# Kernel tuning notes

Measured on AMD Instinct MI355X. Metric: run time of the kernel, lower is better.

The kernel has to match this reference:

```python
import jax, jax.numpy as jnp
import numpy as np

IN_FEATURES = 1024
OUT_FEATURES = 1024
BATCH = 32
SEQ = 1024
EPS = 1e-8


def setup_inputs() -> dict:
    key = jax.random.key(0)
    k1, k2, k3 = jax.random.split(key, 3)
    Efou = jax.random.normal(k1, (BATCH, SEQ, IN_FEATURES), dtype=jnp.float32)
    y = jax.random.normal(k2, (BATCH, IN_FEATURES), dtype=jnp.float32)
    weight = jax.random.normal(k3, (IN_FEATURES, OUT_FEATURES), dtype=jnp.float32)
    return {"Efou": Efou, "y": y, "weight": weight}


def reference(Efou, y, weight):
    # scale = 1/sqrt(in_features)
    scale = 1.0 / np.sqrt(np.float32(weight.shape[0]))
    ys = y * scale  # (b, i) == per-sample column scaling of weight
    # Demodulation norm: sum_i (scale*W[i,o]*y[b,i])^2 = (ys^2) @ (W^2)
    d = jax.lax.rsqrt(jnp.einsum('bi,io->bo', ys * ys, weight * weight) + EPS)  # (b, o)
    # Efou @ (scale*W*y*d) == ((Efou*ys) @ W) * d  -- same math, avoids (b,i,o) weight
    out = jnp.einsum('bsi,io->bso', Efou * ys[:, None, :], weight) * d[:, None, :]
    return out
```

## Files before the change

kernel.cpp:

```cpp
#include <hip/hip_runtime.h>

#define AS1 __attribute__((address_space(1)))
#define AS3 __attribute__((address_space(3)))

typedef __bf16 bf16x8 __attribute__((ext_vector_type(8)));
typedef float f32x4 __attribute__((ext_vector_type(4)));
typedef unsigned short ushort8 __attribute__((ext_vector_type(8)));

__device__ __forceinline__ unsigned short f2bf(float f) {
  union { float f; unsigned u; } v; v.f = f;
  unsigned u = v.u;
  unsigned r = (u + 0x7fffu + ((u >> 16) & 1u)) >> 16;
  return (unsigned short)r;
}

__global__ __launch_bounds__(256) void prep_kernel(const float* __restrict__ y,
                                                   const float* __restrict__ W,
                                                   float* __restrict__ partial,
                                                   unsigned short* __restrict__ WT) {
  __shared__ float ysq[32][32];
  const int o = blockIdx.x * 256 + threadIdx.x;
  const int i0 = blockIdx.y * 32;
  for (int e = threadIdx.x; e < 1024; e += 256) {
    int il = e >> 5, b = e & 31;
    float t = y[b * 1024 + i0 + il] * 0.03125f;
    ysq[il][b] = t * t;
  }
  __syncthreads();

  f32x4 acc[8] = {};
  ushort8 wb[4];
#pragma unroll
  for (int il = 0; il < 32; ++il) {
    float w = W[(size_t)(i0 + il) * 1024 + o];
    wb[il >> 3][il & 7] = f2bf(w);
    float w2 = w * w;
#pragma unroll
    for (int b4 = 0; b4 < 8; ++b4) {
      f32x4 q = *(const f32x4*)&ysq[il][b4 * 4];
#pragma unroll
      for (int k = 0; k < 4; ++k) acc[b4][k] = fmaf(q[k], w2, acc[b4][k]);
    }
  }
  unsigned short* wt = WT + (size_t)o * 1024 + i0;
#pragma unroll
  for (int q = 0; q < 4; ++q) *(ushort8*)(wt + q * 8) = wb[q];
  float* p = partial + (size_t)blockIdx.y * 32768 + o;
#pragma unroll
  for (int b4 = 0; b4 < 8; ++b4)
#pragma unroll
    for (int k = 0; k < 4; ++k) p[(b4 * 4 + k) * 1024] = acc[b4][k];
}

__global__ __launch_bounds__(256) void dcalc_b_kernel(const float* __restrict__ partial,
                                                      float* __restrict__ dmod) {
  const int bo = blockIdx.x * 256 + threadIdx.x;
  float acc = 0.f;
#pragma unroll 8
  for (int is = 0; is < 32; ++is) acc += partial[(size_t)is * 32768 + bo];
  dmod[bo] = rsqrtf(acc + 1e-8f);
}

#define NT 16
#define LDS_TILE 65536

#define BAR __builtin_amdgcn_s_barrier()
#define LGKM0 asm volatile("s_waitcnt lgkmcnt(0)" ::: "memory")
#define VM(n) asm volatile("s_waitcnt vmcnt(" #n ")" ::: "memory")
#define SCHB __builtin_amdgcn_sched_barrier(0)
#define PRIO(x) __builtin_amdgcn_s_setprio(x)

#define STG_B(r, t, dst)                                                     \
  __builtin_amdgcn_global_load_lds(                                          \
      (const AS1 void*)(Ws + (size_t)(r) * 64 * 2048 + (t) * 128),           \
      (AS3 void*)((dst) + 32768 + (r) * 8192 + sldso), 16, 0, 0)

#define A_ISSUE(t)                                                           \
  {                                                                          \
    const float* asrc = Efou + (size_t)(m0 + argp * 4) * 1024 + (t) * 64 + k8; \
    _Pragma("unroll") for (int rr = 0; rr < 4; ++rr) {                       \
      pa[rr][0] = *(const f32x4*)(asrc + rr * 1024);                         \
      pa[rr][1] = *(const f32x4*)(asrc + rr * 1024 + 4);                     \
    }                                                                        \
    yv[0] = *(const f32x4*)(ysS + (t) * 64 + k8);                            \
    yv[1] = *(const f32x4*)(ysS + (t) * 64 + k8 + 4);                        \
  }

#define ACVT_ROW(dst, rr)                                                    \
  {                                                                          \
    const int row = argp * 4 + (rr);                                         \
    bf16x8 ov;                                                               \
    _Pragma("unroll") for (int q = 0; q < 4; ++q) {                          \
      ov[q] = (__bf16)(pa[rr][0][q] * yv[0][q]);                             \
      ov[q + 4] = (__bf16)(pa[rr][1][q] * yv[1][q]);                         \
    }                                                                        \
    *(bf16x8*)((dst) + row * 128 + ((kslot * 16) ^ ((row & 7) << 4))) = ov;  \
  }

#define RD_A(mh, mi, kk)                                                     \
  (*(const bf16x8*)(Ab + (wr * 128 + ((mh) * 4 + (mi)) * 16 + l15) * 128 +   \
                    ((((kk) * 64 + lhi * 16)) ^ swz_rd)))
#define RD_B(nh, ni, kk)                                                     \
  (*(const bf16x8*)(Bb + (wc * 64 + ((nh) * 2 + (ni)) * 16 + l15) * 128 +    \
                    ((((kk) * 64 + lhi * 16)) ^ swz_rd)))

#define LD_A(mh)                                                             \
  { _Pragma("unroll") for (int mi = 0; mi < 4; ++mi)                         \
      _Pragma("unroll") for (int kk = 0; kk < 2; ++kk)                       \
        a[mi][kk] = RD_A(mh, mi, kk); }
#define LD_B_ALL                                                             \
  { _Pragma("unroll") for (int nh = 0; nh < 2; ++nh)                         \
      _Pragma("unroll") for (int ni = 0; ni < 2; ++ni)                       \
        _Pragma("unroll") for (int kk = 0; kk < 2; ++kk)                     \
          bfr[nh][ni][kk] = RD_B(nh, ni, kk); }

#define MM(mh, nh)                                                           \
  do {                                                                       \
    _Pragma("unroll") for (int mi = 0; mi < 4; ++mi)                         \
      _Pragma("unroll") for (int ni = 0; ni < 2; ++ni)                       \
        _Pragma("unroll") for (int kk = 0; kk < 2; ++kk)                     \
          acc[(mh) * 4 + mi][(nh) * 2 + ni] =                                \
              __builtin_amdgcn_mfma_f32_16x16x32_bf16(                       \
                  a[mi][kk], bfr[nh][ni][kk],                                \
                  acc[(mh) * 4 + mi][(nh) * 2 + ni], 0, 0, 0);               \
  } while (0)

__global__ __launch_bounds__(512, 2) void gemmf6_kernel(
    const float* __restrict__ Efou, const float* __restrict__ y,
    const unsigned short* __restrict__ WT, const float* __restrict__ dmod,
    float* __restrict__ out) {
  extern __shared__ char lds[];
  float* ysS = (float*)(lds + 2 * LDS_TILE);

  const int tid = threadIdx.x;
  const int bid = blockIdx.x;
  const int wg = (bid & 7) * 64 + (bid >> 3);
  const int bm = wg >> 2, bn = wg & 3;
  const int m0 = bm * 256, n0 = bn * 256;
  const int b = m0 >> 10;

  const int w = tid >> 6, l = tid & 63;
  const int wr = w >> 2, wc = w & 3;
  const int l15 = l & 15, lhi = l >> 4;
  const int swz_rd = (l15 & 7) << 4;

  const int kslot = tid & 7;
  const int k8 = kslot * 8;
  const int argp = tid >> 3;

  const int srow = tid >> 3;
  const int scb = ((tid & 7) << 4) ^ ((srow & 7) << 4);
  const char* Ws = (const char*)WT + (size_t)(n0 + srow) * 2048 + scb;
  const int sldso = tid * 16;

  f32x4 acc[8][4] = {};
  bf16x8 a[4][2], bfr[2][2][2];
  f32x4 pa[4][2], yv[2];

  {
    float2 yy = *(const float2*)(y + b * 1024 + tid * 2);
    ysS[2 * tid] = yy.x * 0.03125f;
    ysS[2 * tid + 1] = yy.y * 0.03125f;
  }
  __syncthreads();
  {
    char* d0 = lds;
    STG_B(0, 0, d0); STG_B(1, 0, d0); STG_B(2, 0, d0); STG_B(3, 0, d0);
    A_ISSUE(0);
    ACVT_ROW(d0, 0); ACVT_ROW(d0, 1); ACVT_ROW(d0, 2); ACVT_ROW(d0, 3);
  }
  VM(0); LGKM0; BAR;

  for (int t = 0; t < NT - 1; ++t) {
    const char* Ab = lds + (t & 1) * LDS_TILE;
    const char* Bb = Ab + 32768;
    char* dN = lds + ((t & 1) ^ 1) * LDS_TILE;
    const int t1 = t + 1;
    LD_A(0); LD_B_ALL;
    A_ISSUE(t1);
    STG_B(0, t1, dN); STG_B(1, t1, dN); STG_B(2, t1, dN); STG_B(3, t1, dN);
    BAR; LGKM0; SCHB; PRIO(1); MM(0, 0); MM(0, 1); PRIO(0); SCHB; BAR;
    LD_A(1);
    SCHB; PRIO(1);
    ACVT_ROW(dN, 0); ACVT_ROW(dN, 1);
    MM(1, 0);
    ACVT_ROW(dN, 2); ACVT_ROW(dN, 3);
    MM(1, 1);
    PRIO(0); SCHB;
    VM(0);
    LGKM0;
    BAR;
  }

  {
    const char* Ab = lds + ((NT - 1) & 1) * LDS_TILE;
    const char* Bb = Ab + 32768;
    LD_A(0); LD_B_ALL;
    BAR; LGKM0; SCHB; PRIO(1); MM(0, 0); MM(0, 1); PRIO(0); SCHB;
    LD_A(1);
    LGKM0; SCHB; PRIO(1); MM(1, 0); MM(1, 1); PRIO(0); SCHB;
  }

  const int col0 = n0 + wc * 64 + l15;
  float dv[4];
#pragma unroll
  for (int nf = 0; nf < 4; ++nf) dv[nf] = dmod[b * 1024 + col0 + nf * 16];
#pragma unroll
  for (int mf = 0; mf < 8; ++mf) {
#pragma unroll
    for (int j = 0; j < 4; ++j) {
      const int row = m0 + wr * 128 + mf * 16 + lhi * 4 + j;
      float* orow = out + (size_t)row * 1024 + col0;
#pragma unroll
      for (int nf = 0; nf < 4; ++nf) orow[nf * 16] = acc[mf][nf][j] * dv[nf];
    }
  }
}

extern "C" void kernel_launch(void* const* d_in, const int* in_sizes, int n_in,
                              void* d_out, int out_size, void* d_ws, size_t ws_size,
                              hipStream_t stream) {
  const float* Efou = (const float*)d_in[0];
  const float* y    = (const float*)d_in[1];
  const float* W    = (const float*)d_in[2];
  float* out = (float*)d_out;

  unsigned short* WT = (unsigned short*)d_ws;
  float* dpart       = (float*)(WT + (size_t)1024 * 1024);
  float* dmod        = dpart + (size_t)32 * 32768;

  hipFuncSetAttribute((const void*)gemmf6_kernel,
                      hipFuncAttributeMaxDynamicSharedMemorySize, 135168);

  prep_kernel<<<dim3(4, 32), 256, 0, stream>>>(y, W, dpart, WT);
  dcalc_b_kernel<<<128, 256, 0, stream>>>(dpart, dmod);
  gemmf6_kernel<<<512, 512, 135168, stream>>>(Efou, y, WT, dmod, out);
}
```

Baseline: 130.2 us.

## Shrink GEMM tile to 128x128 with 256-thread blocks and simpler pipeline

Replaces the 256x256 output tile with 512 threads by a 128x128 tile with 256 threads and 2048 blocks, halving LDS per block. The hand-tuned interleaved schedule (split MFMA halves, sched barriers, extra barrier) becomes a single uniform loop that loads fragments, converts the next A tile, then runs all MFMAs. The aim is more blocks resident per CU and better load balance across CUs. The cost is that each Efou and W element is reloaded twice as often, and less global-load latency is hidden by the simpler schedule.

```diff
diff --git a/kernel.cpp b/kernel.cpp
--- a/kernel.cpp
+++ b/kernel.cpp
@@ -62,18 +62,17 @@
 }
 
 #define NT 16
-#define LDS_TILE 65536
+#define BUFSZ 32768
 
 #define BAR __builtin_amdgcn_s_barrier()
 #define LGKM0 asm volatile("s_waitcnt lgkmcnt(0)" ::: "memory")
 #define VM(n) asm volatile("s_waitcnt vmcnt(" #n ")" ::: "memory")
-#define SCHB __builtin_amdgcn_sched_barrier(0)
 #define PRIO(x) __builtin_amdgcn_s_setprio(x)
 
 #define STG_B(r, t, dst)                                                     \
   __builtin_amdgcn_global_load_lds(                                          \
-      (const AS1 void*)(Ws + (size_t)(r) * 64 * 2048 + (t) * 128),           \
-      (AS3 void*)((dst) + 32768 + (r) * 8192 + sldso), 16, 0, 0)
+      (const AS1 void*)(Ws + (size_t)(r) * 32 * 2048 + (t) * 128),           \
+      (AS3 void*)((dst) + 16384 + (r) * 4096 + tid * 16), 16, 0, 0)
 
 #define A_ISSUE(t)                                                           \
   {                                                                          \
@@ -97,50 +96,29 @@
     *(bf16x8*)((dst) + row * 128 + ((kslot * 16) ^ ((row & 7) << 4))) = ov;  \
   }
 
-#define RD_A(mh, mi, kk)                                                     \
-  (*(const bf16x8*)(Ab + (wr * 128 + ((mh) * 4 + (mi)) * 16 + l15) * 128 +   \
+#define RD_A(mi, kk)                                                         \
+  (*(const bf16x8*)(Ab + (wr * 64 + (mi) * 16 + l15) * 128 +                 \
                     ((((kk) * 64 + lhi * 16)) ^ swz_rd)))
-#define RD_B(nh, ni, kk)                                                     \
-  (*(const bf16x8*)(Bb + (wc * 64 + ((nh) * 2 + (ni)) * 16 + l15) * 128 +    \
+#define RD_B(nf, kk)                                                         \
+  (*(const bf16x8*)(Bb + (wc * 64 + (nf) * 16 + l15) * 128 +                 \
                     ((((kk) * 64 + lhi * 16)) ^ swz_rd)))
 
-#define LD_A(mh)                                                             \
-  { _Pragma("unroll") for (int mi = 0; mi < 4; ++mi)                         \
-      _Pragma("unroll") for (int kk = 0; kk < 2; ++kk)                       \
-        a[mi][kk] = RD_A(mh, mi, kk); }
-#define LD_B_ALL                                                             \
-  { _Pragma("unroll") for (int nh = 0; nh < 2; ++nh)                         \
-      _Pragma("unroll") for (int ni = 0; ni < 2; ++ni)                       \
-        _Pragma("unroll") for (int kk = 0; kk < 2; ++kk)                     \
-          bfr[nh][ni][kk] = RD_B(nh, ni, kk); }
-
-#define MM(mh, nh)                                                           \
-  do {                                                                       \
-    _Pragma("unroll") for (int mi = 0; mi < 4; ++mi)                         \
-      _Pragma("unroll") for (int ni = 0; ni < 2; ++ni)                       \
-        _Pragma("unroll") for (int kk = 0; kk < 2; ++kk)                     \
-          acc[(mh) * 4 + mi][(nh) * 2 + ni] =                                \
-              __builtin_amdgcn_mfma_f32_16x16x32_bf16(                       \
-                  a[mi][kk], bfr[nh][ni][kk],                                \
-                  acc[(mh) * 4 + mi][(nh) * 2 + ni], 0, 0, 0);               \
-  } while (0)
-
-__global__ __launch_bounds__(512, 2) void gemmf6_kernel(
+__global__ __launch_bounds__(256, 2) void gemmf7_kernel(
     const float* __restrict__ Efou, const float* __restrict__ y,
     const unsigned short* __restrict__ WT, const float* __restrict__ dmod,
     float* __restrict__ out) {
   extern __shared__ char lds[];
-  float* ysS = (float*)(lds + 2 * LDS_TILE);
+  float* ysS = (float*)(lds + 2 * BUFSZ);
 
   const int tid = threadIdx.x;
   const int bid = blockIdx.x;
-  const int wg = (bid & 7) * 64 + (bid >> 3);
-  const int bm = wg >> 2, bn = wg & 3;
-  const int m0 = bm * 256, n0 = bn * 256;
+  const int wg = (bid & 7) * 256 + (bid >> 3);
+  const int bm = wg >> 3, bn = wg & 7;
+  const int m0 = bm * 128, n0 = bn * 128;
   const int b = m0 >> 10;
 
   const int w = tid >> 6, l = tid & 63;
-  const int wr = w >> 2, wc = w & 3;
+  const int wr = w >> 1, wc = w & 1;
   const int l15 = l & 15, lhi = l >> 4;
   const int swz_rd = (l15 & 7) << 4;
 
@@ -151,16 +129,17 @@
   const int srow = tid >> 3;
   const int scb = ((tid & 7) << 4) ^ ((srow & 7) << 4);
   const char* Ws = (const char*)WT + (size_t)(n0 + srow) * 2048 + scb;
-  const int sldso = tid * 16;
-
-  f32x4 acc[8][4] = {};
-  bf16x8 a[4][2], bfr[2][2][2];
+
+  f32x4 acc[4][4] = {};
+  bf16x8 a[4][2], bfr[4][2];
   f32x4 pa[4][2], yv[2];
 
   {
-    float2 yy = *(const float2*)(y + b * 1024 + tid * 2);
-    ysS[2 * tid] = yy.x * 0.03125f;
-    ysS[2 * tid + 1] = yy.y * 0.03125f;
+    f32x4 yy = *(const f32x4*)(y + b * 1024 + tid * 4);
+    ysS[4 * tid] = yy[0] * 0.03125f;
+    ysS[4 * tid + 1] = yy[1] * 0.03125f;
+    ysS[4 * tid + 2] = yy[2] * 0.03125f;
+    ysS[4 * tid + 3] = yy[3] * 0.03125f;
   }
   __syncthreads();
   {
@@ -171,48 +150,53 @@
   }
   VM(0); LGKM0; BAR;
 
-  for (int t = 0; t < NT - 1; ++t) {
-    const char* Ab = lds + (t & 1) * LDS_TILE;
-    const char* Bb = Ab + 32768;
-    char* dN = lds + ((t & 1) ^ 1) * LDS_TILE;
-    const int t1 = t + 1;
-    LD_A(0); LD_B_ALL;
-    A_ISSUE(t1);
-    STG_B(0, t1, dN); STG_B(1, t1, dN); STG_B(2, t1, dN); STG_B(3, t1, dN);
-    BAR; LGKM0; SCHB; PRIO(1); MM(0, 0); MM(0, 1); PRIO(0); SCHB; BAR;
-    LD_A(1);
-    SCHB; PRIO(1);
-    ACVT_ROW(dN, 0); ACVT_ROW(dN, 1);
-    MM(1, 0);
-    ACVT_ROW(dN, 2); ACVT_ROW(dN, 3);
-    MM(1, 1);
-    PRIO(0); SCHB;
-    VM(0);
+  for (int t = 0; t < NT; ++t) {
+    const char* Ab = lds + (t & 1) * BUFSZ;
+    const char* Bb = Ab + 16384;
+    char* dN = lds + ((t + 1) & 1) * BUFSZ;
+    if (t < NT - 1) {
+      A_ISSUE(t + 1);
+      STG_B(0, t + 1, dN); STG_B(1, t + 1, dN);
+      STG_B(2, t + 1, dN); STG_B(3, t + 1, dN);
+    }
+#pragma unroll
+    for (int mi = 0; mi < 4; ++mi)
+#pragma unroll
+      for (int kk = 0; kk < 2; ++kk) a[mi][kk] = RD_A(mi, kk);
+#pragma unroll
+    for (int nf = 0; nf < 4; ++nf)
+#pragma unroll
+      for (int kk = 0; kk < 2; ++kk) bfr[nf][kk] = RD_B(nf, kk);
+    if (t < NT - 1) {
+      ACVT_ROW(dN, 0); ACVT_ROW(dN, 1); ACVT_ROW(dN, 2); ACVT_ROW(dN, 3);
+    }
+    PRIO(1);
+#pragma unroll
+    for (int mi = 0; mi < 4; ++mi)
+#pragma unroll
+      for (int nf = 0; nf < 4; ++nf)
+#pragma unroll
+        for (int kk = 0; kk < 2; ++kk)
+          acc[mi][nf] = __builtin_amdgcn_mfma_f32_16x16x32_bf16(
+              a[mi][kk], bfr[nf][kk], acc[mi][nf], 0, 0, 0);
+    PRIO(0);
+    if (t < NT - 1) { VM(0); }
     LGKM0;
     BAR;
   }
 
-  {
-    const char* Ab = lds + ((NT - 1) & 1) * LDS_TILE;
-    const char* Bb = Ab + 32768;
-    LD_A(0); LD_B_ALL;
-    BAR; LGKM0; SCHB; PRIO(1); MM(0, 0); MM(0, 1); PRIO(0); SCHB;
-    LD_A(1);
-    LGKM0; SCHB; PRIO(1); MM(1, 0); MM(1, 1); PRIO(0); SCHB;
-  }
-
   const int col0 = n0 + wc * 64 + l15;
   float dv[4];
 #pragma unroll
   for (int nf = 0; nf < 4; ++nf) dv[nf] = dmod[b * 1024 + col0 + nf * 16];
 #pragma unroll
-  for (int mf = 0; mf < 8; ++mf) {
+  for (int mi = 0; mi < 4; ++mi) {
 #pragma unroll
     for (int j = 0; j < 4; ++j) {
-      const int row = m0 + wr * 128 + mf * 16 + lhi * 4 + j;
+      const int row = m0 + wr * 64 + mi * 16 + lhi * 4 + j;
       float* orow = out + (size_t)row * 1024 + col0;
 #pragma unroll
-      for (int nf = 0; nf < 4; ++nf) orow[nf * 16] = acc[mf][nf][j] * dv[nf];
+      for (int nf = 0; nf < 4; ++nf) orow[nf * 16] = acc[mi][nf][j] * dv[nf];
     }
   }
 }
@@ -229,10 +213,10 @@
   float* dpart       = (float*)(WT + (size_t)1024 * 1024);
   float* dmod        = dpart + (size_t)32 * 32768;
 
-  hipFuncSetAttribute((const void*)gemmf6_kernel,
-                      hipFuncAttributeMaxDynamicSharedMemorySize, 135168);
+  hipFuncSetAttribute((const void*)gemmf7_kernel,
+                      hipFuncAttributeMaxDynamicSharedMemorySize, 69632);
 
   prep_kernel<<<dim3(4, 32), 256, 0, stream>>>(y, W, dpart, WT);
   dcalc_b_kernel<<<128, 256, 0, stream>>>(dpart, dmod);
-  gemmf6_kernel<<<512, 512, 135168, stream>>>(Efou, y, WT, dmod, out);
-}
+  gemmf7_kernel<<<2048, 256, 69632, stream>>>(Efou, y, WT, dmod, out);
+}
```

After: 141.5 us. +8.7%, slower.
